# Kernel tuning notes

Hardware: AMD Instinct MI355X
Metric: run time of the kernel (lower is better)

The kernel has to match this reference:

```python
import jax, jax.numpy as jnp
import numpy as np

B, S, D, H, HS, FF, L, V = 8, 512, 512, 8, 64, 2048, 6, 1024
EPS = 1e-5


def _layer_norm(x, g, b):
    m = jnp.mean(x, axis=-1, keepdims=True)
    v = jnp.var(x, axis=-1, keepdims=True)
    return (x - m) * jax.lax.rsqrt(v + EPS) * g + b


def _pos_encoding(seq_len, d, dtype):
    # Faithful to source: exponent uses 2*i/seq_len (x.shape[seq_dim]), not d_model.
    pos = jnp.arange(seq_len, dtype=dtype)[:, None]
    i = jnp.arange(d)
    pe = pos / (10000.0 ** (2.0 * i.astype(dtype) / seq_len))
    return jnp.where(i % 2 == 0, jnp.sin(pe), jnp.cos(pe))


def setup_inputs() -> dict:
    key = jax.random.key(0)
    ks = jax.random.split(key, 16)
    tok_ids = jax.random.randint(ks[0], (B, S), 0, V)
    tokens = jax.nn.one_hot(tok_ids, V, dtype=jnp.float32)
    std = 0.02
    return {
        "tokens": tokens,
        "token_embeddings": jax.random.normal(ks[1], (V, D), jnp.float32),
        "qkv_w": jax.random.normal(ks[2], (L, H, D, 3 * HS), jnp.float32) * std,
        "qkv_b": jnp.zeros((L, H, 3 * HS), jnp.float32),
        "out_w": jax.random.normal(ks[3], (L, D, D), jnp.float32) * std,
        "out_b": jnp.zeros((L, D), jnp.float32),
        "w1": jax.random.normal(ks[4], (L, D, FF), jnp.float32) * std,
        "b1": jnp.zeros((L, FF), jnp.float32),
        "w2": jax.random.normal(ks[5], (L, FF, D), jnp.float32) * std,
        "b2": jnp.zeros((L, D), jnp.float32),
        "ln1_g": jnp.ones((L, D), jnp.float32),
        "ln1_b": jnp.zeros((L, D), jnp.float32),
        "ln2_g": jnp.ones((L, D), jnp.float32),
        "ln2_b": jnp.zeros((L, D), jnp.float32),
    }


def _forward(tokens, token_embeddings, qkv_w, qkv_b, out_w, out_b,
             w1, b1, w2, b2, ln1_g, ln1_b, ln2_g, ln2_b):
    dt = tokens.dtype
    x = tokens @ (token_embeddings * (D ** 0.5))          # [B,S,D]
    x = x + _pos_encoding(S, D, dt)
    # Multiplicative causal mask (faithful to source: -1e6 strictly above diag, 0 elsewhere)
    mask = jnp.triu(jnp.full((S, S), -1e6, dt), k=1)
    scale = 1.0 / (HS ** 0.5)

    def block(x, p):
        (qw, qb, ow, ob, w1_, b1_, w2_, b2_, g1, be1, g2, be2) = p
        qkv = jnp.einsum('bsd,hdk->bhsk', x, qw) + qb[None, :, None, :]
        q, k, v = jnp.split(qkv, 3, axis=-1)              # each [B,H,S,HS]
        logits = jnp.einsum('bhsk,bhtk->bhst', q, k)      # [B,H,S,S]
        attn = jax.nn.softmax(logits * mask * scale, axis=-1)
        o = jnp.einsum('bhst,bhtk->bhsk', attn, v)
        o = o.transpose(0, 2, 1, 3).reshape(x.shape[0], S, D)  # concat heads
        o = o @ ow + ob
        x = _layer_norm(x + o, g1, be1)
        h = jax.nn.relu(x @ w1_ + b1_) @ w2_ + b2_
        x = _layer_norm(x + h, g2, be2)
        return x, None

    params = (qkv_w, qkv_b, out_w, out_b, w1, b1, w2, b2, ln1_g, ln1_b, ln2_g, ln2_b)
    x, _ = jax.lax.scan(block, x, params)
    return x @ token_embeddings.T                          # [B,S,V]


def reference(tokens, token_embeddings, qkv_w, qkv_b, out_w, out_b,
              w1, b1, w2, b2, ln1_g, ln1_b, ln2_g, ln2_b):
    return _forward(tokens, token_embeddings, qkv_w, qkv_b, out_w, out_b,
                    w1, b1, w2, b2, ln1_g, ln1_b, ln2_g, ln2_b)
```

## Files before the change

### kernel.cpp

```cpp
#include <hip/hip_runtime.h>
#include <math.h>

#define BB 8
#define SS 512
#define DD 512
#define HH 8
#define HSD 64
#define FFD 2048
#define LL 6
#define VV 1024
#define NROWS (BB*SS)
#define EPS 1e-5f

__global__ __launch_bounds__(256)
void embed_kernel(const float* __restrict__ tokens,
                  const float* __restrict__ emb,
                  float* __restrict__ x)
{
    const int n = blockIdx.x;
    const int s = n & (SS - 1);
    const int t = threadIdx.x;
    __shared__ int sidx;
    #pragma unroll
    for (int r = 0; r < 4; ++r) {
        int v = t + 256 * r;
        if (tokens[(long)n * VV + v] > 0.5f) sidx = v;
    }
    __syncthreads();
    const int idx = sidx;
    const float sq = 22.62741699796952f;
    #pragma unroll
    for (int r = 0; r < 2; ++r) {
        int d = t + 256 * r;
        float e = emb[(long)idx * DD + d] * sq;
        float expo  = (2.0f * (float)d) / 512.0f;
        float denom = powf(10000.0f, expo);
        float val   = (float)s / denom;
        float pe = ((d & 1) == 0) ? sinf(val) : cosf(val);
        x[(long)n * DD + d] = e + pe;
    }
}

template<int TNB, bool BT, bool QKVB, bool BIAS, bool RELU, bool RES>
__global__ __launch_bounds__(256)
void gemm_t(const float* __restrict__ A, const float* __restrict__ B,
            const float* __restrict__ bias, const float* __restrict__ res,
            float* __restrict__ C,
            int M, int N, int K, int lda, int ldb, int ldc)
{
    constexpr int NW  = TNB / 16;
    constexpr int BSH = (TNB == 128) ? 5 : 4;
    const int t  = threadIdx.x;
    const int bm = blockIdx.y * 128;
    const int bn = blockIdx.x * TNB;
    __shared__ float As[32][132];
    __shared__ float Bs[32][TNB + 4];
    const int tx = t & 15;
    const int ty = t >> 4;
    float acc[8][NW] = {};

    for (int k0 = 0; k0 < K; k0 += 32) {
        #pragma unroll
        for (int p = 0; p < 4; ++p) {
            int q = t + 256 * p;
            int r = q >> 3, kc = (q & 7) * 4;
            float4 a4 = *(const float4*)(A + (long)(bm + r) * lda + k0 + kc);
            As[kc + 0][r] = a4.x; As[kc + 1][r] = a4.y;
            As[kc + 2][r] = a4.z; As[kc + 3][r] = a4.w;
        }
        if (QKVB) {
            #pragma unroll
            for (int p = 0; p < TNB / 32; ++p) {
                int q = t + 256 * p;
                int r = q >> BSH, c = (q & ((1 << BSH) - 1)) * 4;
                int col = bn + c;
                int h = (int)((unsigned)col / 192u);
                int j = col - h * 192;
                *(float4*)&Bs[r][c] =
                    *(const float4*)(B + (long)h * (DD * 192) + (long)(k0 + r) * 192 + j);
            }
        } else if (!BT) {
            #pragma unroll
            for (int p = 0; p < TNB / 32; ++p) {
                int q = t + 256 * p;
                int r = q >> BSH, c = (q & ((1 << BSH) - 1)) * 4;
                *(float4*)&Bs[r][c] = *(const float4*)(B + (long)(k0 + r) * ldb + bn + c);
            }
        } else {
            #pragma unroll
            for (int p = 0; p < TNB / 32; ++p) {
                int q = t + 256 * p;
                int r = q >> 3, kc = (q & 7) * 4;
                float4 b4 = *(const float4*)(B + (long)(bn + r) * ldb + k0 + kc);
                Bs[kc + 0][r] = b4.x; Bs[kc + 1][r] = b4.y;
                Bs[kc + 2][r] = b4.z; Bs[kc + 3][r] = b4.w;
            }
        }
        __syncthreads();
        #pragma unroll
        for (int kk = 0; kk < 32; ++kk) {
            float a[8], bv[NW];
            *(float4*)&a[0] = *(const float4*)&As[kk][ty * 8];
            *(float4*)&a[4] = *(const float4*)&As[kk][ty * 8 + 4];
            #pragma unroll
            for (int g = 0; g < NW / 4; ++g)
                *(float4*)&bv[g * 4] = *(const float4*)&Bs[kk][tx * NW + g * 4];
            #pragma unroll
            for (int ii = 0; ii < 8; ++ii)
                #pragma unroll
                for (int jj = 0; jj < NW; ++jj)
                    acc[ii][jj] += a[ii] * bv[jj];
        }
        __syncthreads();
    }

    #pragma unroll
    for (int ii = 0; ii < 8; ++ii) {
        int r = bm + ty * 8 + ii;
        #pragma unroll
        for (int jj = 0; jj < NW; ++jj) {
            int c = bn + tx * NW + jj;
            float v = acc[ii][jj];
            if (BIAS) v += bias[c];
            if (RELU) v = fmaxf(v, 0.0f);
            if (RES)  v += res[(long)r * ldc + c];
            C[(long)r * ldc + c] = v;
        }
    }
}

__device__ __forceinline__ void gll16(const float* g, float* l)
{
    __builtin_amdgcn_global_load_lds(
        (const __attribute__((address_space(1))) void*)g,
        (__attribute__((address_space(3))) void*)l, 16, 0, 0);
}

__global__ __launch_bounds__(256)
void attn_kernel(const float* __restrict__ qkv, float* __restrict__ oc)
{
    const int i0 = blockIdx.x * 16;
    const int h  = blockIdx.y, b = blockIdx.z;
    const int t  = threadIdx.x;
    const int w  = t >> 6;
    const int ln = t & 63;

    __shared__ __align__(16) float Qs[16][64];
    __shared__ __align__(16) float KV[2][64 * 64];
    __shared__ __align__(16) float Zb[16][512];

    const float* __restrict__ base = qkv + (long)b * SS * 1536 + (long)h * 192;

    const int rB = ln >> 4;
    const int g0 = ln & 15;
    const int gx = g0 ^ rB;

    gll16(base + (long)(i0 + 4 * w + rB) * 1536 + g0 * 4, &Qs[4 * w][0]);
    #pragma unroll
    for (int p = 0; p < 4; ++p) {
        int q = 4 * w + p;
        int r = 4 * q + rB;
        int g = (gx ^ (p << 2)) << 2;
        gll16(base + (long)r * 1536 + 64 + g, &KV[0][q * 256]);
    }
    __syncthreads();

    for (int kt = 0; kt < 8; ++kt) {
        const int cur = kt & 1;
        float* nb = &KV[cur ^ 1][0];
        if (kt < 7) {
            const int j0n = (kt + 1) * 64;
            #pragma unroll
            for (int p = 0; p < 4; ++p) {
                int q = 4 * w + p;
                int r = 4 * q + rB;
                int g = (gx ^ (p << 2)) << 2;
                gll16(base + (long)(j0n + r) * 1536 + 64 + g, nb + q * 256);
            }
        } else {
            #pragma unroll
            for (int p = 0; p < 4; ++p) {
                int q = 4 * w + p;
                int r = 4 * q + rB;
                gll16(base + (long)r * 1536 + 128 + g0 * 4, nb + q * 256);
            }
        }

        const float* cb = &KV[cur][0];
        float4 kreg[16];
        #pragma unroll
        for (int kk = 0; kk < 16; ++kk)
            kreg[kk] = *(const float4*)(cb + ln * 64 + ((kk ^ g0) << 2));

        const int j0 = kt * 64;
        #pragma unroll
        for (int c = 0; c < 4; ++c) {
            const int i = 4 * w + c;
            const float4* q4 = (const float4*)&Qs[i][0];
            float dot = 0.0f;
            #pragma unroll
            for (int kk = 0; kk < 16; ++kk) {
                float4 kv = kreg[kk];
                float4 qq = q4[kk];
                dot += qq.x * kv.x + qq.y * kv.y + qq.z * kv.z + qq.w * kv.w;
            }
            const int gi = i0 + i, gj = j0 + ln;
            Zb[i][j0 + ln] = (gj <= gi) ? 0.0f : (dot * -1.0e6f) * 0.125f;
        }
        __syncthreads();
    }

    #pragma unroll
    for (int c = 0; c < 4; ++c) {
        const int i = 4 * w + c;
        float p[8];
        float mx = -3.4e38f;
        #pragma unroll
        for (int r = 0; r < 8; ++r) { p[r] = Zb[i][r * 64 + ln]; mx = fmaxf(mx, p[r]); }
        #pragma unroll
        for (int o = 32; o >= 1; o >>= 1) mx = fmaxf(mx, __shfl_xor(mx, o));
        float sum = 0.0f;
        #pragma unroll
        for (int r = 0; r < 8; ++r) { p[r] = expf(p[r] - mx); sum += p[r]; }
        #pragma unroll
        for (int o = 32; o >= 1; o >>= 1) sum += __shfl_xor(sum, o);
        const float inv = 1.0f / sum;
        #pragma unroll
        for (int r = 0; r < 8; ++r) Zb[i][r * 64 + ln] = p[r] * inv;
    }

    float oA[4] = {0.0f, 0.0f, 0.0f, 0.0f};
    for (int kt = 0; kt < 8; ++kt) {
        const int cur = kt & 1;
        if (kt < 7) {
            float* nb = &KV[cur ^ 1][0];
            const int j0n = (kt + 1) * 64;
            #pragma unroll
            for (int p = 0; p < 4; ++p) {
                int q = 4 * w + p;
                int r = 4 * q + rB;
                gll16(base + (long)(j0n + r) * 1536 + 128 + g0 * 4, nb + q * 256);
            }
        }

        const float* cb = &KV[cur][0];
        float vreg[64];
        #pragma unroll
        for (int kk = 0; kk < 64; ++kk) vreg[kk] = cb[kk * 64 + ln];

        const int j0 = kt * 64;
        #pragma unroll
        for (int c = 0; c < 4; ++c) {
            const int i = 4 * w + c;
            const float4* pr = (const float4*)&Zb[i][j0];
            float acc = oA[c];
            #pragma unroll
            for (int kk = 0; kk < 16; ++kk) {
                float4 pv = pr[kk];
                acc += pv.x * vreg[kk * 4 + 0];
                acc += pv.y * vreg[kk * 4 + 1];
                acc += pv.z * vreg[kk * 4 + 2];
                acc += pv.w * vreg[kk * 4 + 3];
            }
            oA[c] = acc;
        }
        if (kt < 7) __syncthreads();
    }

    #pragma unroll
    for (int c = 0; c < 4; ++c) {
        const int gi = i0 + 4 * w + c;
        oc[(long)(b * SS + gi) * DD + h * HSD + ln] = oA[c];
    }
}

__device__ __forceinline__ float blk_sum(float v, float* sb)
{
    #pragma unroll
    for (int m = 32; m >= 1; m >>= 1) v += __shfl_xor(v, m);
    if ((threadIdx.x & 63) == 0) sb[threadIdx.x >> 6] = v;
    __syncthreads();
    v = sb[0] + sb[1] + sb[2] + sb[3];
    __syncthreads();
    return v;
}

__global__ __launch_bounds__(256)
void ln_kernel(const float* __restrict__ in, const float* __restrict__ g,
               const float* __restrict__ bb, float* __restrict__ out)
{
    __shared__ float sb[4];
    const int n = blockIdx.x;
    const int t = threadIdx.x;
    const float* x = in + (long)n * DD;
    float v0 = x[t], v1 = x[t + 256];
    float total = blk_sum(v0 + v1, sb);
    float mean = total * (1.0f / 512.0f);
    float d0 = v0 - mean, d1 = v1 - mean;
    float ss = blk_sum(d0 * d0 + d1 * d1, sb);
    float var = ss * (1.0f / 512.0f);
    float inv = 1.0f / sqrtf(var + EPS);
    out[(long)n * DD + t]       = d0 * inv * g[t]       + bb[t];
    out[(long)n * DD + t + 256] = d1 * inv * g[t + 256] + bb[t + 256];
}

extern "C" void kernel_launch(void* const* d_in, const int* in_sizes, int n_in,
                              void* d_out, int out_size, void* d_ws, size_t ws_size,
                              hipStream_t stream)
{
    const float* tokens = (const float*)d_in[0];
    const float* emb    = (const float*)d_in[1];
    const float* qkv_w  = (const float*)d_in[2];
    const float* qkv_b  = (const float*)d_in[3];
    const float* out_w  = (const float*)d_in[4];
    const float* out_b  = (const float*)d_in[5];
    const float* w1     = (const float*)d_in[6];
    const float* b1     = (const float*)d_in[7];
    const float* w2     = (const float*)d_in[8];
    const float* b2     = (const float*)d_in[9];
    const float* ln1_g  = (const float*)d_in[10];
    const float* ln1_b  = (const float*)d_in[11];
    const float* ln2_g  = (const float*)d_in[12];
    const float* ln2_b  = (const float*)d_in[13];
    float* out = (float*)d_out;

    float* ws  = (float*)d_ws;
    float* x   = ws;
    float* y   = x  + (long)NROWS * DD;
    float* oc  = y  + (long)NROWS * DD;
    float* big = oc + (long)NROWS * DD;

    embed_kernel<<<NROWS, 256, 0, stream>>>(tokens, emb, x);

    for (int l = 0; l < LL; ++l) {
        const float* qw  = qkv_w + (long)l * HH * DD * 192;
        const float* qb  = qkv_b + (long)l * HH * 192;
        const float* ow  = out_w + (long)l * DD * DD;
        const float* ob  = out_b + (long)l * DD;
        const float* w1l = w1 + (long)l * DD * FFD;
        const float* b1l = b1 + (long)l * FFD;
        const float* w2l = w2 + (long)l * FFD * DD;
        const float* b2l = b2 + (long)l * DD;

        gemm_t<64, false, true, true, false, false><<<dim3(24, 32), 256, 0, stream>>>(
            x, qw, qb, nullptr, big, NROWS, 1536, DD, DD, 192, 1536);

        attn_kernel<<<dim3(SS / 16, HH, BB), 256, 0, stream>>>(big, oc);

        gemm_t<64, false, false, true, false, true><<<dim3(8, 32), 256, 0, stream>>>(
            oc, ow, ob, x, y, NROWS, DD, DD, DD, DD, DD);

        ln_kernel<<<NROWS, 256, 0, stream>>>(y, ln1_g + (long)l * DD, ln1_b + (long)l * DD, x);

        gemm_t<128, false, false, true, true, false><<<dim3(16, 32), 256, 0, stream>>>(
            x, w1l, b1l, nullptr, big, NROWS, FFD, DD, DD, FFD, FFD);

        gemm_t<64, false, false, true, false, true><<<dim3(8, 32), 256, 0, stream>>>(
            big, w2l, b2l, x, y, NROWS, DD, FFD, FFD, DD, DD);

        ln_kernel<<<NROWS, 256, 0, stream>>>(y, ln2_g + (long)l * DD, ln2_b + (long)l * DD, x);
    }

    gemm_t<64, true, false, false, false, false><<<dim3(16, 32), 256, 0, stream>>>(
        x, emb, nullptr, nullptr, out, NROWS, VV, DD, DD, DD, VV);
}
```

Baseline: 3.890 ms.

## Remap GEMM threads to one row per thread; keep attention scores in registers

The GEMM thread mapping changes from an 8xNW register tile per thread to one output row with TNB/2 columns per thread. B values become wave-wide LDS broadcast reads, and the epilogue uses float4 bias, residual and output accesses. In the attention kernel, the 16x512 shared score buffer is replaced by per-thread registers plus a small per-wave probability staging buffer, and the K/V register loads are split into halves. This cuts attention LDS use and may allow higher occupancy. The cost is many more LDS read instructions per FMA in the GEMM, output stores that are strided across rows, and higher register pressure from the 64-element accumulator.

```diff
diff --git a/kernel.cpp b/kernel.cpp
--- a/kernel.cpp
+++ b/kernel.cpp
@@ -48,16 +48,18 @@
             float* __restrict__ C,
             int M, int N, int K, int lda, int ldb, int ldc)
 {
-    constexpr int NW  = TNB / 16;
+    constexpr int NW  = TNB / 2;
     constexpr int BSH = (TNB == 128) ? 5 : 4;
     const int t  = threadIdx.x;
+    const int w  = t >> 6;
+    const int ln = t & 63;
     const int bm = blockIdx.y * 128;
     const int bn = blockIdx.x * TNB;
     __shared__ float As[32][132];
-    __shared__ float Bs[32][TNB + 4];
-    const int tx = t & 15;
-    const int ty = t >> 4;
-    float acc[8][NW] = {};
+    __shared__ __align__(16) float Bs[32][TNB + 4];
+    const int rw = (w >> 1) * 64 + ln;
+    const int c0 = (w & 1) * NW;
+    float acc[NW] = {};
 
     for (int k0 = 0; k0 < K; k0 += 32) {
         #pragma unroll
@@ -99,33 +101,39 @@
         __syncthreads();
         #pragma unroll
         for (int kk = 0; kk < 32; ++kk) {
-            float a[8], bv[NW];
-            *(float4*)&a[0] = *(const float4*)&As[kk][ty * 8];
-            *(float4*)&a[4] = *(const float4*)&As[kk][ty * 8 + 4];
-            #pragma unroll
-            for (int g = 0; g < NW / 4; ++g)
-                *(float4*)&bv[g * 4] = *(const float4*)&Bs[kk][tx * NW + g * 4];
-            #pragma unroll
-            for (int ii = 0; ii < 8; ++ii)
-                #pragma unroll
-                for (int jj = 0; jj < NW; ++jj)
-                    acc[ii][jj] += a[ii] * bv[jj];
+            float a = As[kk][rw];
+            #pragma unroll
+            for (int g = 0; g < NW / 4; ++g) {
+                float4 b4 = *(const float4*)&Bs[kk][c0 + g * 4];
+                acc[g * 4 + 0] += a * b4.x;
+                acc[g * 4 + 1] += a * b4.y;
+                acc[g * 4 + 2] += a * b4.z;
+                acc[g * 4 + 3] += a * b4.w;
+            }
         }
         __syncthreads();
     }
 
-    #pragma unroll
-    for (int ii = 0; ii < 8; ++ii) {
-        int r = bm + ty * 8 + ii;
-        #pragma unroll
-        for (int jj = 0; jj < NW; ++jj) {
-            int c = bn + tx * NW + jj;
-            float v = acc[ii][jj];
-            if (BIAS) v += bias[c];
-            if (RELU) v = fmaxf(v, 0.0f);
-            if (RES)  v += res[(long)r * ldc + c];
-            C[(long)r * ldc + c] = v;
-        }
+    const int r = bm + rw;
+    #pragma unroll
+    for (int g = 0; g < NW / 4; ++g) {
+        int c = bn + c0 + g * 4;
+        float4 v;
+        v.x = acc[g * 4 + 0]; v.y = acc[g * 4 + 1];
+        v.z = acc[g * 4 + 2]; v.w = acc[g * 4 + 3];
+        if (BIAS) {
+            v.x += bias[c + 0]; v.y += bias[c + 1];
+            v.z += bias[c + 2]; v.w += bias[c + 3];
+        }
+        if (RELU) {
+            v.x = fmaxf(v.x, 0.0f); v.y = fmaxf(v.y, 0.0f);
+            v.z = fmaxf(v.z, 0.0f); v.w = fmaxf(v.w, 0.0f);
+        }
+        if (RES) {
+            float4 r4 = *(const float4*)(res + (long)r * ldc + c);
+            v.x += r4.x; v.y += r4.y; v.z += r4.z; v.w += r4.w;
+        }
+        *(float4*)(C + (long)r * ldc + c) = v;
     }
 }
 
@@ -147,7 +155,7 @@
 
     __shared__ __align__(16) float Qs[16][64];
     __shared__ __align__(16) float KV[2][64 * 64];
-    __shared__ __align__(16) float Zb[16][512];
+    __shared__ __align__(16) float Pb[4][4][64];
 
     const float* __restrict__ base = qkv + (long)b * SS * 1536 + (long)h * 192;
 
@@ -165,6 +173,9 @@
     }
     __syncthreads();
 
+    float s[4][8];
+
+    #pragma unroll
     for (int kt = 0; kt < 8; ++kt) {
         const int cur = kt & 1;
         float* nb = &KV[cur ^ 1][0];
@@ -187,36 +198,41 @@
         }
 
         const float* cb = &KV[cur][0];
-        float4 kreg[16];
-        #pragma unroll
-        for (int kk = 0; kk < 16; ++kk)
-            kreg[kk] = *(const float4*)(cb + ln * 64 + ((kk ^ g0) << 2));
-
-        const int j0 = kt * 64;
+        float dots[4] = {0.0f, 0.0f, 0.0f, 0.0f};
+        #pragma unroll
+        for (int hf = 0; hf < 2; ++hf) {
+            float4 kreg[8];
+            #pragma unroll
+            for (int kk = 0; kk < 8; ++kk)
+                kreg[kk] = *(const float4*)(cb + ln * 64 + (((hf * 8 + kk) ^ g0) << 2));
+            #pragma unroll
+            for (int c = 0; c < 4; ++c) {
+                const int i = 4 * w + c;
+                const float4* q4 = (const float4*)&Qs[i][0];
+                float dot = dots[c];
+                #pragma unroll
+                for (int kk = 0; kk < 8; ++kk) {
+                    float4 kv = kreg[kk];
+                    float4 qq = q4[hf * 8 + kk];
+                    dot += qq.x * kv.x + qq.y * kv.y + qq.z * kv.z + qq.w * kv.w;
+                }
+                dots[c] = dot;
+            }
+        }
         #pragma unroll
         for (int c = 0; c < 4; ++c) {
-            const int i = 4 * w + c;
-            const float4* q4 = (const float4*)&Qs[i][0];
-            float dot = 0.0f;
-            #pragma unroll
-            for (int kk = 0; kk < 16; ++kk) {
-                float4 kv = kreg[kk];
-                float4 qq = q4[kk];
-                dot += qq.x * kv.x + qq.y * kv.y + qq.z * kv.z + qq.w * kv.w;
-            }
-            const int gi = i0 + i, gj = j0 + ln;
-            Zb[i][j0 + ln] = (gj <= gi) ? 0.0f : (dot * -1.0e6f) * 0.125f;
+            const int gi = i0 + 4 * w + c, gj = kt * 64 + ln;
+            s[c][kt] = (gj <= gi) ? 0.0f : (dots[c] * -1.0e6f) * 0.125f;
         }
         __syncthreads();
     }
 
     #pragma unroll
     for (int c = 0; c < 4; ++c) {
-        const int i = 4 * w + c;
         float p[8];
         float mx = -3.4e38f;
         #pragma unroll
-        for (int r = 0; r < 8; ++r) { p[r] = Zb[i][r * 64 + ln]; mx = fmaxf(mx, p[r]); }
+        for (int r = 0; r < 8; ++r) { p[r] = s[c][r]; mx = fmaxf(mx, p[r]); }
         #pragma unroll
         for (int o = 32; o >= 1; o >>= 1) mx = fmaxf(mx, __shfl_xor(mx, o));
         float sum = 0.0f;
@@ -226,10 +242,11 @@
         for (int o = 32; o >= 1; o >>= 1) sum += __shfl_xor(sum, o);
         const float inv = 1.0f / sum;
         #pragma unroll
-        for (int r = 0; r < 8; ++r) Zb[i][r * 64 + ln] = p[r] * inv;
+        for (int r = 0; r < 8; ++r) s[c][r] = p[r] * inv;
     }
 
     float oA[4] = {0.0f, 0.0f, 0.0f, 0.0f};
+    #pragma unroll
     for (int kt = 0; kt < 8; ++kt) {
         const int cur = kt & 1;
         if (kt < 7) {
@@ -243,26 +260,30 @@
             }
         }
 
+        #pragma unroll
+        for (int c = 0; c < 4; ++c) Pb[w][c][ln] = s[c][kt];
+
         const float* cb = &KV[cur][0];
-        float vreg[64];
-        #pragma unroll
-        for (int kk = 0; kk < 64; ++kk) vreg[kk] = cb[kk * 64 + ln];
-
-        const int j0 = kt * 64;
-        #pragma unroll
-        for (int c = 0; c < 4; ++c) {
-            const int i = 4 * w + c;
-            const float4* pr = (const float4*)&Zb[i][j0];
-            float acc = oA[c];
-            #pragma unroll
-            for (int kk = 0; kk < 16; ++kk) {
-                float4 pv = pr[kk];
-                acc += pv.x * vreg[kk * 4 + 0];
-                acc += pv.y * vreg[kk * 4 + 1];
-                acc += pv.z * vreg[kk * 4 + 2];
-                acc += pv.w * vreg[kk * 4 + 3];
-            }
-            oA[c] = acc;
+        #pragma unroll
+        for (int hf = 0; hf < 2; ++hf) {
+            float vreg[32];
+            #pragma unroll
+            for (int kk = 0; kk < 32; ++kk)
+                vreg[kk] = cb[(hf * 32 + kk) * 64 + ln];
+            #pragma unroll
+            for (int c = 0; c < 4; ++c) {
+                const float4* pr = (const float4*)&Pb[w][c][hf * 32];
+                float acc = oA[c];
+                #pragma unroll
+                for (int kk = 0; kk < 8; ++kk) {
+                    float4 pv = pr[kk];
+                    acc += pv.x * vreg[kk * 4 + 0];
+                    acc += pv.y * vreg[kk * 4 + 1];
+                    acc += pv.z * vreg[kk * 4 + 2];
+                    acc += pv.w * vreg[kk * 4 + 3];
+                }
+                oA[c] = acc;
+            }
         }
         if (kt < 7) __syncthreads();
     }
```

After: 7.987 ms. +105.3%, slower.
